# Performance work log

Hardware: AMD Instinct MI355X
Metric: run time of the kernel (lower is better)

## Reference

```python
import jax, jax.numpy as jnp
import numpy as np

DIM = 128       # model dim d
NEXP = 64       # number of experts
K = 2           # top-k (hardcoded in the module)
B, S = 1, 1024  # batch, seq
HID = DIM * 4   # expert FFN hidden = 4*d


def _gelu(v):
    # torch F.gelu / nn.GELU default = exact erf form
    return jax.nn.gelu(v, approximate=False)


def setup_inputs() -> dict:
    key = jax.random.key(0)
    ks = jax.random.split(key, 8)
    sc = 0.02
    xav = (2.0 / (HID + DIM)) ** 0.5  # xavier_normal std for [4d, d]
    x = jax.random.normal(ks[0], (B, S, DIM), jnp.float32)
    # gate MLP: Linear(d,4d) -> GELU -> Linear(4d,4d) -> GELU -> Linear(4d,E) -> Sigmoid
    gw1 = jax.random.normal(ks[1], (DIM, HID), jnp.float32) * sc
    gb1 = jnp.zeros((HID,), jnp.float32)
    gw2 = jax.random.normal(ks[2], (HID, HID), jnp.float32) * sc
    gb2 = jnp.zeros((HID,), jnp.float32)
    gw3 = jax.random.normal(ks[3], (HID, NEXP), jnp.float32) * sc
    gb3 = jnp.zeros((NEXP,), jnp.float32)
    # expert banks (shapes fixed to the consistent 2-layer FFN reading)
    W1 = jax.random.normal(ks[4], (NEXP, HID, DIM), jnp.float32) * xav
    B1 = jnp.zeros((NEXP, HID), jnp.float32)
    W2 = jax.random.normal(ks[5], (NEXP, DIM, HID), jnp.float32) * xav
    B2 = jnp.zeros((NEXP, DIM), jnp.float32)
    return dict(x=x, gw1=gw1, gb1=gb1, gw2=gw2, gb2=gb2, gw3=gw3, gb3=gb3,
                W1=W1, B1=B1, W2=W2, B2=B2)


def reference(x, gw1, gb1, gw2, gb2, gw3, gb3, W1, B1, W2, B2):
    # gating network -> sigmoid scores over experts
    h = _gelu(x @ gw1 + gb1)
    h = _gelu(h @ gw2 + gb2)
    gate = jax.nn.sigmoid(h @ gw3 + gb3)                 # [B,S,E]
    values, idx = jax.lax.top_k(gate, K)                 # [B,S,K]
    values = values / jnp.sum(values, axis=-1, keepdims=True)
    # naive per-token gather of full expert weights (matches original access pattern)
    w1g = W1[idx]                                        # [B,S,K,HID,DIM]
    b1g = B1[idx]                                        # [B,S,K,HID]
    w2g = W2[idx]                                        # [B,S,K,DIM,HID]
    b2g = B2[idx]                                        # [B,S,K,DIM]
    t = _gelu(jnp.einsum('bskfd,bsd->bskf', w1g, x) + b1g)   # [B,S,K,HID]
    y = _gelu(jnp.einsum('bskdf,bskf->bskd', w2g, t) + b2g)  # [B,S,K,DIM]
    return jnp.sum(y * values[..., None], axis=-2)           # [B,S,DIM]
```

## Files before the change

### kernel.cpp

```cpp
#include <hip/hip_runtime.h>
#include <math.h>

#define NDIM 128
#define NHID 512
#define NEXPERT 64
#define NTOK 1024
#define NPAIR (NTOK * 2)

typedef __attribute__((ext_vector_type(8))) short short8_t;
typedef __attribute__((ext_vector_type(4))) float f32x4;

__device__ __forceinline__ float gelu_f(float v) {
    return 0.5f * v * (1.0f + erff(v * 0.7071067811865476f));
}
__device__ __forceinline__ unsigned short f2bf(float f) {
    union { float f; unsigned u; } v; v.f = f;
    unsigned r = v.u + 0x7FFFu + ((v.u >> 16) & 1u);
    return (unsigned short)(r >> 16);
}
__device__ __forceinline__ float bf2f(unsigned short h) {
    union { unsigned u; float f; } v; v.u = ((unsigned)h) << 16;
    return v.f;
}
__device__ __forceinline__ void split3(float f, short& ho, short& mo, short& lo) {
    const unsigned short h = f2bf(f);
    const float r1 = f - bf2f(h);
    const unsigned short m = f2bf(r1);
    const unsigned short l = f2bf(r1 - bf2f(m));
    ho = (short)h; mo = (short)m; lo = (short)l;
}

__global__ __launch_bounds__(256) void k_g1d2(
        const float* __restrict__ x, const float* __restrict__ gw1,
        const float* __restrict__ gw2, const float* __restrict__ gb1,
        unsigned short* __restrict__ G2h, unsigned short* __restrict__ G2m,
        unsigned short* __restrict__ G2l, unsigned short* __restrict__ Hh,
        unsigned short* __restrict__ Hm, unsigned short* __restrict__ Hl) {
    __shared__ __align__(16) char smem[58112];
    const int j = threadIdx.x;
    if (blockIdx.x >= 256) {
        float (*T)[65] = (float (*)[65])smem;
        const int u = blockIdx.x - 256;
        const int k0 = (u >> 3) * 64, n0 = (u & 7) * 64;
#pragma unroll
        for (int q = 0; q < 4; ++q) {
            const int idx = j + 256 * q;
            const int kr = idx >> 4, c4 = idx & 15;
            float4 v = *(const float4*)(gw2 + (size_t)(k0 + kr) * NHID + n0 + c4 * 4);
            T[kr][c4 * 4 + 0] = v.x; T[kr][c4 * 4 + 1] = v.y;
            T[kr][c4 * 4 + 2] = v.z; T[kr][c4 * 4 + 3] = v.w;
        }
        __syncthreads();
#pragma unroll
        for (int q = 0; q < 4; ++q) {
            const int idx = j + 256 * q;
            const int n = idx >> 4, k4 = idx & 15;
            short4 sh, sm, sl;
#pragma unroll
            for (int qq = 0; qq < 4; ++qq)
                split3(T[k4 * 4 + qq][n], (&sh.x)[qq], (&sm.x)[qq], (&sl.x)[qq]);
            const size_t o = (size_t)(n0 + n) * NHID + k0 + k4 * 4;
            *(short4*)(G2h + o) = sh;
            *(short4*)(G2m + o) = sm;
            *(short4*)(G2l + o) = sl;
        }
        return;
    }
    short (*Ahs)[32][72] = (short (*)[32][72])smem;
    short (*Bss)[64][72] = (short (*)[64][72])(smem + 13824);
    float (*T)[65] = (float (*)[65])(smem + 41472);
    const int u = blockIdx.x;
    const int m0 = (u >> 3) * 32, n0 = (u & 7) * 64;
    const int w = j >> 6, lane = j & 63;
    const int mt = w & 1, npair = w >> 1;
    const int lrow = lane & 15, lseg = lane >> 4;
    f32x4 acc[2];
    acc[0] = (f32x4){0.f, 0.f, 0.f, 0.f};
    acc[1] = (f32x4){0.f, 0.f, 0.f, 0.f};
    for (int kc = 0; kc < NDIM; kc += 64) {
        __syncthreads();
#pragma unroll
        for (int q = 0; q < 4; ++q) {
            const int idx = j + 256 * q;
            const int kr = idx >> 4, c4 = idx & 15;
            float4 v = *(const float4*)(gw1 + (size_t)(kc + kr) * NHID + n0 + c4 * 4);
            T[kr][c4 * 4 + 0] = v.x; T[kr][c4 * 4 + 1] = v.y;
            T[kr][c4 * 4 + 2] = v.z; T[kr][c4 * 4 + 3] = v.w;
        }
#pragma unroll
        for (int q = 0; q < 2; ++q) {
            const int idx = j + 256 * q;
            const int row = idx >> 4, c4 = idx & 15;
            float4 v = *(const float4*)(x + (size_t)(m0 + row) * NDIM + kc + c4 * 4);
            short4 sh, sm, sl;
#pragma unroll
            for (int qq = 0; qq < 4; ++qq)
                split3((&v.x)[qq], (&sh.x)[qq], (&sm.x)[qq], (&sl.x)[qq]);
            *(short4*)&Ahs[0][row][c4 * 4] = sh;
            *(short4*)&Ahs[1][row][c4 * 4] = sm;
            *(short4*)&Ahs[2][row][c4 * 4] = sl;
        }
        __syncthreads();
#pragma unroll
        for (int q = 0; q < 4; ++q) {
            const int idx = j + 256 * q;
            const int nn = idx >> 4, k4 = idx & 15;
            short4 sh, sm, sl;
#pragma unroll
            for (int qq = 0; qq < 4; ++qq)
                split3(T[k4 * 4 + qq][nn], (&sh.x)[qq], (&sm.x)[qq], (&sl.x)[qq]);
            *(short4*)&Bss[0][nn][k4 * 4] = sh;
            *(short4*)&Bss[1][nn][k4 * 4] = sm;
            *(short4*)&Bss[2][nn][k4 * 4] = sl;
        }
        __syncthreads();
#pragma unroll
        for (int ks = 0; ks < 2; ++ks) {
            const int ko = ks * 32 + lseg * 8;
            short8_t ah = *(short8_t*)&Ahs[0][mt * 16 + lrow][ko];
            short8_t am = *(short8_t*)&Ahs[1][mt * 16 + lrow][ko];
            short8_t al = *(short8_t*)&Ahs[2][mt * 16 + lrow][ko];
#pragma unroll
            for (int nt = 0; nt < 2; ++nt) {
                const int nr = (npair * 2 + nt) * 16 + lrow;
                short8_t bh = *(short8_t*)&Bss[0][nr][ko];
                short8_t bm = *(short8_t*)&Bss[1][nr][ko];
                short8_t bl = *(short8_t*)&Bss[2][nr][ko];
                acc[nt] = __builtin_amdgcn_mfma_f32_16x16x32_bf16(ah, bh, acc[nt], 0, 0, 0);
                acc[nt] = __builtin_amdgcn_mfma_f32_16x16x32_bf16(am, bh, acc[nt], 0, 0, 0);
                acc[nt] = __builtin_amdgcn_mfma_f32_16x16x32_bf16(ah, bm, acc[nt], 0, 0, 0);
                acc[nt] = __builtin_amdgcn_mfma_f32_16x16x32_bf16(al, bh, acc[nt], 0, 0, 0);
                acc[nt] = __builtin_amdgcn_mfma_f32_16x16x32_bf16(ah, bl, acc[nt], 0, 0, 0);
                acc[nt] = __builtin_amdgcn_mfma_f32_16x16x32_bf16(am, bm, acc[nt], 0, 0, 0);
            }
        }
    }
#pragma unroll
    for (int nt = 0; nt < 2; ++nt) {
        const int col = n0 + (npair * 2 + nt) * 16 + lrow;
        const float bb = gb1[col];
#pragma unroll
        for (int r = 0; r < 4; ++r) {
            const int row = m0 + mt * 16 + lseg * 4 + r;
            const float h = gelu_f(acc[nt][r] + bb);
            short hh, hm, hl;
            split3(h, hh, hm, hl);
            const size_t o = (size_t)row * NHID + col;
            Hh[o] = (unsigned short)hh; Hm[o] = (unsigned short)hm;
            Hl[o] = (unsigned short)hl;
        }
    }
}

__global__ __launch_bounds__(256) void k_gate2(
        const unsigned short* __restrict__ Ahp, const unsigned short* __restrict__ Amp,
        const unsigned short* __restrict__ Alp,
        const unsigned short* __restrict__ Bhp, const unsigned short* __restrict__ Bmp,
        const unsigned short* __restrict__ Blp,
        const float* __restrict__ gb2, float* __restrict__ h2) {
    __shared__ short Ahs[3][32][72];
    __shared__ short Bss[3][64][72];
    const int j = threadIdx.x;
    const int u = blockIdx.x;
    const int m0 = (u >> 3) * 32, n0 = (u & 7) * 64;
    const int w = j >> 6, lane = j & 63;
    const int mt = w & 1, npair = w >> 1;
    const int lrow = lane & 15, lseg = lane >> 4;
    const int K = NHID;
    f32x4 acc[2];
    acc[0] = (f32x4){0.f, 0.f, 0.f, 0.f};
    acc[1] = (f32x4){0.f, 0.f, 0.f, 0.f};
    for (int kc = 0; kc < K; kc += 64) {
        __syncthreads();
        {
            const int row = j >> 3, c8 = j & 7;
            const size_t o = (size_t)(m0 + row) * K + kc + c8 * 8;
            *(short8_t*)&Ahs[0][row][c8 * 8] = *(const short8_t*)(Ahp + o);
            *(short8_t*)&Ahs[1][row][c8 * 8] = *(const short8_t*)(Amp + o);
            *(short8_t*)&Ahs[2][row][c8 * 8] = *(const short8_t*)(Alp + o);
        }
#pragma unroll
        for (int q = 0; q < 2; ++q) {
            const int idx = j + 256 * q;
            const int nr = idx >> 3, c8 = idx & 7;
            const size_t o = (size_t)(n0 + nr) * K + kc + c8 * 8;
            *(short8_t*)&Bss[0][nr][c8 * 8] = *(const short8_t*)(Bhp + o);
            *(short8_t*)&Bss[1][nr][c8 * 8] = *(const short8_t*)(Bmp + o);
            *(short8_t*)&Bss[2][nr][c8 * 8] = *(const short8_t*)(Blp + o);
        }
        __syncthreads();
#pragma unroll
        for (int ks = 0; ks < 2; ++ks) {
            const int ko = ks * 32 + lseg * 8;
            short8_t ah = *(short8_t*)&Ahs[0][mt * 16 + lrow][ko];
            short8_t am = *(short8_t*)&Ahs[1][mt * 16 + lrow][ko];
            short8_t al = *(short8_t*)&Ahs[2][mt * 16 + lrow][ko];
#pragma unroll
            for (int nt = 0; nt < 2; ++nt) {
                const int nr = (npair * 2 + nt) * 16 + lrow;
                short8_t bh = *(short8_t*)&Bss[0][nr][ko];
                short8_t bm = *(short8_t*)&Bss[1][nr][ko];
                short8_t bl = *(short8_t*)&Bss[2][nr][ko];
                acc[nt] = __builtin_amdgcn_mfma_f32_16x16x32_bf16(ah, bh, acc[nt], 0, 0, 0);
                acc[nt] = __builtin_amdgcn_mfma_f32_16x16x32_bf16(am, bh, acc[nt], 0, 0, 0);
                acc[nt] = __builtin_amdgcn_mfma_f32_16x16x32_bf16(ah, bm, acc[nt], 0, 0, 0);
                acc[nt] = __builtin_amdgcn_mfma_f32_16x16x32_bf16(al, bh, acc[nt], 0, 0, 0);
                acc[nt] = __builtin_amdgcn_mfma_f32_16x16x32_bf16(ah, bl, acc[nt], 0, 0, 0);
                acc[nt] = __builtin_amdgcn_mfma_f32_16x16x32_bf16(am, bm, acc[nt], 0, 0, 0);
            }
        }
    }
#pragma unroll
    for (int nt = 0; nt < 2; ++nt) {
        const int col = n0 + (npair * 2 + nt) * 16 + lrow;
        const float bb = gb2[col];
#pragma unroll
        for (int r = 0; r < 4; ++r) {
            const int row = m0 + mt * 16 + lseg * 4 + r;
            h2[(size_t)row * NHID + col] = gelu_f(acc[nt][r] + bb);
        }
    }
}

__global__ __launch_bounds__(256) void k_gate3(
        const float* __restrict__ h2, const float* __restrict__ gw3,
        const float* __restrict__ gb3, int* __restrict__ eidx,
        float* __restrict__ wval) {
    __shared__ float hs[8][132];
    __shared__ float gs[128][72];
    const int j = threadIdx.x;
    const int lane = j & 63;
    const int w = j >> 6;
    const int t0 = blockIdx.x * 8;
    float acc[2] = {0.f, 0.f};
    for (int k0 = 0; k0 < NHID; k0 += 128) {
        __syncthreads();
        {
            const int tok = j >> 5, c4 = j & 31;
            *(float4*)&hs[tok][c4 * 4] =
                *(const float4*)(h2 + (size_t)(t0 + tok) * NHID + k0 + c4 * 4);
        }
#pragma unroll
        for (int q = 0; q < 8; ++q) {
            const int idx = j + 256 * q;
            const int kk = idx >> 4, c4 = idx & 15;
            *(float4*)&gs[kk][c4 * 4] =
                *(const float4*)(gw3 + (size_t)(k0 + kk) * NEXPERT + c4 * 4);
        }
        __syncthreads();
        for (int kk = 0; kk < 128; ++kk) {
            const float g = gs[kk][lane];
            acc[0] += hs[w * 2][kk] * g;
            acc[1] += hs[w * 2 + 1][kk] * g;
        }
    }
    const float bias = gb3[lane];
#pragma unroll
    for (int i = 0; i < 2; ++i) {
        const int t = t0 + w * 2 + i;
        float s = 1.f / (1.f + expf(-(acc[i] + bias)));
        float v = s; int ix = lane;
#pragma unroll
        for (int off = 32; off >= 1; off >>= 1) {
            float ov = __shfl_xor(v, off);
            int oi = __shfl_xor(ix, off);
            if (ov > v || (ov == v && oi < ix)) { v = ov; ix = oi; }
        }
        const float v0 = v; const int i0 = ix;
        float v2 = (lane == i0) ? -1.f : s; int ix2 = lane;
#pragma unroll
        for (int off = 32; off >= 1; off >>= 1) {
            float ov = __shfl_xor(v2, off);
            int oi = __shfl_xor(ix2, off);
            if (ov > v2 || (ov == v2 && oi < ix2)) { v2 = ov; ix2 = oi; }
        }
        if (lane == 0) {
            float inv = 1.f / (v0 + v2);
            eidx[t * 2] = i0;  eidx[t * 2 + 1] = ix2;
            wval[t * 2] = v0 * inv;  wval[t * 2 + 1] = v2 * inv;
        }
    }
}

__device__ __forceinline__ int build_list(
        const int* __restrict__ eidx, int e, int lane, int w,
        int* lst, int* wtot) {
    unsigned long long msk[8];
    const int b0 = w * 512;
    int tot = 0;
#pragma unroll
    for (int c = 0; c < 8; ++c) {
        const int i = b0 + c * 64 + lane;
        msk[c] = __ballot(eidx[i] == e);
        tot += (int)__popcll(msk[c]);
    }
    if (lane == 0) wtot[w] = tot;
    __syncthreads();
    int woff = 0;
    for (int q = 0; q < w; ++q) woff += wtot[q];
    int run = 0;
#pragma unroll
    for (int c = 0; c < 8; ++c) {
        const int i = b0 + c * 64 + lane;
        if ((msk[c] >> lane) & 1ull)
            lst[woff + run + (int)__popcll(msk[c] & ((1ull << lane) - 1ull))] = i;
        run += (int)__popcll(msk[c]);
    }
    const int n = wtot[0] + wtot[1] + wtot[2] + wtot[3];
    __syncthreads();
    return n;
}

__global__ __launch_bounds__(256) void k_l1(
        const float* __restrict__ x, const float* __restrict__ W1,
        const float* __restrict__ B1, const int* __restrict__ eidx,
        unsigned short* __restrict__ tbuf) {
    __shared__ short As_[32 * 136];
    __shared__ short Bs_[64 * 136];
    __shared__ int prs[32];
    __shared__ int wtot[4];
    __shared__ int lst[NPAIR];
    const int j = threadIdx.x;
    const int lane = j & 63;
    const int w = j >> 6;
    const int e = blockIdx.x >> 3;
    const int f0 = (blockIdx.x & 7) * 64;
    char* Asc = (char*)As_;
    char* Bsc = (char*)Bs_;
    const int n = build_list(eidx, e, lane, w, lst, wtot);
    const float* W1e = W1 + (size_t)e * NHID * NDIM;
    for (int idx = j; idx < 2048; idx += 256) {
        const int f = idx >> 5, c4 = idx & 31;
        float4 v = *(const float4*)(W1e + (size_t)(f0 + f) * NDIM + c4 * 4);
        short4 s; s.x = (short)f2bf(v.x); s.y = (short)f2bf(v.y);
        s.z = (short)f2bf(v.z); s.w = (short)f2bf(v.w);
        *(short4*)(Bsc + f * 272 + c4 * 8) = s;
    }
    const float bbias = B1[e * NHID + f0 + w * 16 + (lane & 15)];
    for (int bt = 0; bt * 32 < n; ++bt) {
        __syncthreads();
        if (j < 32) prs[j] = (bt * 32 + j < n) ? lst[bt * 32 + j] : -1;
        __syncthreads();
        for (int idx = j; idx < 1024; idx += 256) {
            const int tok = idx >> 5, c4 = idx & 31;
            const int pr = prs[tok];
            float4 v = make_float4(0.f, 0.f, 0.f, 0.f);
            if (pr >= 0) v = ((const float4*)x)[(size_t)(pr >> 1) * 32 + c4];
            short4 s; s.x = (short)f2bf(v.x); s.y = (short)f2bf(v.y);
            s.z = (short)f2bf(v.z); s.w = (short)f2bf(v.w);
            *(short4*)(Asc + tok * 272 + c4 * 8) = s;
        }
        __syncthreads();
        f32x4 acc[2];
        acc[0] = (f32x4){0.f, 0.f, 0.f, 0.f};
        acc[1] = (f32x4){0.f, 0.f, 0.f, 0.f};
        const int acol = ((lane >> 4) << 4);
        const int brow = w * 16 + (lane & 15);
#pragma unroll
        for (int ks = 0; ks < 4; ++ks) {
            short8_t b = *(short8_t*)(Bsc + brow * 272 + ks * 64 + acol);
#pragma unroll
            for (int mt = 0; mt < 2; ++mt) {
                short8_t a = *(short8_t*)(Asc + (mt * 16 + (lane & 15)) * 272 + ks * 64 + acol);
                acc[mt] = __builtin_amdgcn_mfma_f32_16x16x32_bf16(a, b, acc[mt], 0, 0, 0);
            }
        }
        const int fcol = f0 + w * 16 + (lane & 15);
#pragma unroll
        for (int mt = 0; mt < 2; ++mt) {
#pragma unroll
            for (int r = 0; r < 4; ++r) {
                const int tok = mt * 16 + ((lane >> 4) << 2) + r;
                const int pr = prs[tok];
                if (pr >= 0)
                    tbuf[(size_t)pr * NHID + fcol] = f2bf(gelu_f(acc[mt][r] + bbias));
            }
        }
    }
}

__global__ __launch_bounds__(256) void k_l2(
        const float* __restrict__ W2, const int* __restrict__ eidx,
        const unsigned short* __restrict__ tbuf, float* __restrict__ pbuf) {
    __shared__ short As_[32 * 136];
    __shared__ short Bs_[64 * 136];
    __shared__ int prs[32];
    __shared__ int wtot[4];
    __shared__ int lst[NPAIR];
    const int j = threadIdx.x;
    const int lane = j & 63;
    const int w = j >> 6;
    const int e = blockIdx.x >> 3;
    const int d0 = ((blockIdx.x >> 2) & 1) * 64;
    const int kz = blockIdx.x & 3;
    const int k0 = kz * 128;
    char* Asc = (char*)As_;
    char* Bsc = (char*)Bs_;
    const int n = build_list(eidx, e, lane, w, lst, wtot);
    const float* W2e = W2 + (size_t)e * NDIM * NHID;
    for (int idx = j; idx < 2048; idx += 256) {
        const int d = idx >> 5, c4 = idx & 31;
        float4 v = *(const float4*)(W2e + (size_t)(d0 + d) * NHID + k0 + c4 * 4);
        short4 s; s.x = (short)f2bf(v.x); s.y = (short)f2bf(v.y);
        s.z = (short)f2bf(v.z); s.w = (short)f2bf(v.w);
        *(short4*)(Bsc + d * 272 + c4 * 8) = s;
    }
    float* pz = pbuf + (size_t)kz * NPAIR * NDIM;
    for (int bt = 0; bt * 32 < n; ++bt) {
        __syncthreads();
        if (j < 32) prs[j] = (bt * 32 + j < n) ? lst[bt * 32 + j] : -1;
        __syncthreads();
        for (int idx = j; idx < 512; idx += 256) {
            const int tok = idx >> 4, c8 = idx & 15;
            const int pr = prs[tok];
            short8_t v = (short8_t)(short)0;
            if (pr >= 0) v = *(const short8_t*)(tbuf + (size_t)pr * NHID + k0 + c8 * 8);
            *(short8_t*)(Asc + tok * 272 + c8 * 16) = v;
        }
        __syncthreads();
        f32x4 acc[2];
        acc[0] = (f32x4){0.f, 0.f, 0.f, 0.f};
        acc[1] = (f32x4){0.f, 0.f, 0.f, 0.f};
        const int acol = ((lane >> 4) << 4);
        const int brow = w * 16 + (lane & 15);
#pragma unroll
        for (int ks = 0; ks < 4; ++ks) {
            short8_t b = *(short8_t*)(Bsc + brow * 272 + ks * 64 + acol);
#pragma unroll
            for (int mt = 0; mt < 2; ++mt) {
                short8_t a = *(short8_t*)(Asc + (mt * 16 + (lane & 15)) * 272 + ks * 64 + acol);
                acc[mt] = __builtin_amdgcn_mfma_f32_16x16x32_bf16(a, b, acc[mt], 0, 0, 0);
            }
        }
        const int dcol = d0 + w * 16 + (lane & 15);
#pragma unroll
        for (int mt = 0; mt < 2; ++mt) {
#pragma unroll
            for (int r = 0; r < 4; ++r) {
                const int tok = mt * 16 + ((lane >> 4) << 2) + r;
                const int pr = prs[tok];
                if (pr >= 0) pz[(size_t)pr * NDIM + dcol] = acc[mt][r];
            }
        }
    }
}

__global__ __launch_bounds__(256) void k_combine(
        const float* __restrict__ pbuf, const float* __restrict__ wval,
        const int* __restrict__ eidx, const float* __restrict__ B2,
        float* __restrict__ out) {
    const int i = blockIdx.x * 256 + threadIdx.x;
    const int t = i >> 7, d = i & (NDIM - 1);
    const int KS = NPAIR * NDIM;
    float y[2];
#pragma unroll
    for (int k = 0; k < 2; ++k) {
        const int p = t * 2 + k;
        float s = pbuf[p * NDIM + d] + pbuf[KS + p * NDIM + d]
                + pbuf[2 * KS + p * NDIM + d] + pbuf[3 * KS + p * NDIM + d]
                + B2[eidx[p] * NDIM + d];
        y[k] = gelu_f(s);
    }
    out[i] = wval[t * 2] * y[0] + wval[t * 2 + 1] * y[1];
}

extern "C" void kernel_launch(void* const* d_in, const int* in_sizes, int n_in,
                              void* d_out, int out_size, void* d_ws, size_t ws_size,
                              hipStream_t stream) {
    const float* x   = (const float*)d_in[0];
    const float* gw1 = (const float*)d_in[1];
    const float* gb1 = (const float*)d_in[2];
    const float* gw2 = (const float*)d_in[3];
    const float* gb2 = (const float*)d_in[4];
    const float* gw3 = (const float*)d_in[5];
    const float* gb3 = (const float*)d_in[6];
    const float* W1  = (const float*)d_in[7];
    const float* B1  = (const float*)d_in[8];
    const float* W2  = (const float*)d_in[9];
    const float* B2  = (const float*)d_in[10];
    float* out = (float*)d_out;
    char* ws = (char*)d_ws;

    unsigned short* G2h = (unsigned short*)(ws);
    unsigned short* G2m = (unsigned short*)(ws + 524288);
    unsigned short* G2l = (unsigned short*)(ws + 1048576);
    unsigned short* Hh  = (unsigned short*)(ws + 1572864);
    unsigned short* Hm  = (unsigned short*)(ws + 2621440);
    unsigned short* Hl  = (unsigned short*)(ws + 3670016);
    float*          h2  = (float*)(ws + 4718592);
    unsigned short* tbuf = (unsigned short*)(ws);
    float*          pbuf = (float*)(ws + 2097152);
    int*   eidx = (int*)  (ws + 7340032);
    float* wval = (float*)(ws + 7340032 + 8192);

    k_g1d2<<<dim3(320), 256, 0, stream>>>(x, gw1, gw2, gb1, G2h, G2m, G2l, Hh, Hm, Hl);
    k_gate2<<<dim3(256), 256, 0, stream>>>(Hh, Hm, Hl, G2h, G2m, G2l, gb2, h2);
    k_gate3<<<dim3(128), 256, 0, stream>>>(h2, gw3, gb3, eidx, wval);
    k_l1<<<dim3(512), 256, 0, stream>>>(x, W1, B1, eidx, tbuf);
    k_l2<<<dim3(512), 256, 0, stream>>>(W2, eidx, tbuf, pbuf);
    k_combine<<<dim3(512), 256, 0, stream>>>(pbuf, wval, eidx, B2, out);
}
```

Measured before the change: 62.83 us.

## Fuse expert layer-1 and layer-2 kernels with per-expert spin barrier

```diff
diff --git a/kernel.cpp b/kernel.cpp
--- a/kernel.cpp
+++ b/kernel.cpp
@@ -225,17 +225,18 @@
 __global__ __launch_bounds__(256) void k_gate3(
         const float* __restrict__ h2, const float* __restrict__ gw3,
         const float* __restrict__ gb3, int* __restrict__ eidx,
-        float* __restrict__ wval) {
-    __shared__ float hs[8][132];
+        float* __restrict__ wval, int* __restrict__ cnt) {
+    __shared__ float hs[4][132];
     __shared__ float gs[128][72];
     const int j = threadIdx.x;
     const int lane = j & 63;
     const int w = j >> 6;
-    const int t0 = blockIdx.x * 8;
-    float acc[2] = {0.f, 0.f};
+    const int t0 = blockIdx.x * 4;
+    if (blockIdx.x == 0 && j < NEXPERT) cnt[j] = 0;
+    float acc = 0.f;
     for (int k0 = 0; k0 < NHID; k0 += 128) {
         __syncthreads();
-        {
+        if (j < 128) {
             const int tok = j >> 5, c4 = j & 31;
             *(float4*)&hs[tok][c4 * 4] =
                 *(const float4*)(h2 + (size_t)(t0 + tok) * NHID + k0 + c4 * 4);
@@ -248,17 +249,12 @@
                 *(const float4*)(gw3 + (size_t)(k0 + kk) * NEXPERT + c4 * 4);
         }
         __syncthreads();
-        for (int kk = 0; kk < 128; ++kk) {
-            const float g = gs[kk][lane];
-            acc[0] += hs[w * 2][kk] * g;
-            acc[1] += hs[w * 2 + 1][kk] * g;
-        }
+        for (int kk = 0; kk < 128; ++kk) acc += hs[w][kk] * gs[kk][lane];
     }
     const float bias = gb3[lane];
-#pragma unroll
-    for (int i = 0; i < 2; ++i) {
-        const int t = t0 + w * 2 + i;
-        float s = 1.f / (1.f + expf(-(acc[i] + bias)));
+    {
+        const int t = t0 + w;
+        float s = 1.f / (1.f + expf(-(acc + bias)));
         float v = s; int ix = lane;
 #pragma unroll
         for (int off = 32; off >= 1; off >>= 1) {
@@ -311,10 +307,11 @@
     return n;
 }
 
-__global__ __launch_bounds__(256) void k_l1(
+__global__ __launch_bounds__(256, 2) void k_l1l2(
         const float* __restrict__ x, const float* __restrict__ W1,
-        const float* __restrict__ B1, const int* __restrict__ eidx,
-        unsigned short* __restrict__ tbuf) {
+        const float* __restrict__ B1, const float* __restrict__ W2,
+        const int* __restrict__ eidx, unsigned short* __restrict__ tbuf,
+        float* __restrict__ pbuf, int* __restrict__ cnt) {
     __shared__ short As_[32 * 136];
     __shared__ short Bs_[64 * 136];
     __shared__ int prs[32];
@@ -323,123 +320,122 @@
     const int j = threadIdx.x;
     const int lane = j & 63;
     const int w = j >> 6;
-    const int e = blockIdx.x >> 3;
-    const int f0 = (blockIdx.x & 7) * 64;
+    const int e = blockIdx.x & 63;
+    const int u = blockIdx.x >> 6;
     char* Asc = (char*)As_;
     char* Bsc = (char*)Bs_;
     const int n = build_list(eidx, e, lane, w, lst, wtot);
-    const float* W1e = W1 + (size_t)e * NHID * NDIM;
-    for (int idx = j; idx < 2048; idx += 256) {
-        const int f = idx >> 5, c4 = idx & 31;
-        float4 v = *(const float4*)(W1e + (size_t)(f0 + f) * NDIM + c4 * 4);
-        short4 s; s.x = (short)f2bf(v.x); s.y = (short)f2bf(v.y);
-        s.z = (short)f2bf(v.z); s.w = (short)f2bf(v.w);
-        *(short4*)(Bsc + f * 272 + c4 * 8) = s;
-    }
-    const float bbias = B1[e * NHID + f0 + w * 16 + (lane & 15)];
-    for (int bt = 0; bt * 32 < n; ++bt) {
-        __syncthreads();
-        if (j < 32) prs[j] = (bt * 32 + j < n) ? lst[bt * 32 + j] : -1;
-        __syncthreads();
-        for (int idx = j; idx < 1024; idx += 256) {
-            const int tok = idx >> 5, c4 = idx & 31;
-            const int pr = prs[tok];
-            float4 v = make_float4(0.f, 0.f, 0.f, 0.f);
-            if (pr >= 0) v = ((const float4*)x)[(size_t)(pr >> 1) * 32 + c4];
+
+    {
+        const int f0 = u * 64;
+        const float* W1e = W1 + (size_t)e * NHID * NDIM;
+        for (int idx = j; idx < 2048; idx += 256) {
+            const int f = idx >> 5, c4 = idx & 31;
+            float4 v = *(const float4*)(W1e + (size_t)(f0 + f) * NDIM + c4 * 4);
             short4 s; s.x = (short)f2bf(v.x); s.y = (short)f2bf(v.y);
             s.z = (short)f2bf(v.z); s.w = (short)f2bf(v.w);
-            *(short4*)(Asc + tok * 272 + c4 * 8) = s;
-        }
-        __syncthreads();
-        f32x4 acc[2];
-        acc[0] = (f32x4){0.f, 0.f, 0.f, 0.f};
-        acc[1] = (f32x4){0.f, 0.f, 0.f, 0.f};
-        const int acol = ((lane >> 4) << 4);
-        const int brow = w * 16 + (lane & 15);
-#pragma unroll
-        for (int ks = 0; ks < 4; ++ks) {
-            short8_t b = *(short8_t*)(Bsc + brow * 272 + ks * 64 + acol);
+            *(short4*)(Bsc + f * 272 + c4 * 8) = s;
+        }
+        const float bbias = B1[e * NHID + f0 + w * 16 + (lane & 15)];
+        for (int bt = 0; bt * 32 < n; ++bt) {
+            __syncthreads();
+            if (j < 32) prs[j] = (bt * 32 + j < n) ? lst[bt * 32 + j] : -1;
+            __syncthreads();
+            for (int idx = j; idx < 1024; idx += 256) {
+                const int tok = idx >> 5, c4 = idx & 31;
+                const int pr = prs[tok];
+                float4 v = make_float4(0.f, 0.f, 0.f, 0.f);
+                if (pr >= 0) v = ((const float4*)x)[(size_t)(pr >> 1) * 32 + c4];
+                short4 s; s.x = (short)f2bf(v.x); s.y = (short)f2bf(v.y);
+                s.z = (short)f2bf(v.z); s.w = (short)f2bf(v.w);
+                *(short4*)(Asc + tok * 272 + c4 * 8) = s;
+            }
+            __syncthreads();
+            f32x4 acc[2];
+            acc[0] = (f32x4){0.f, 0.f, 0.f, 0.f};
+            acc[1] = (f32x4){0.f, 0.f, 0.f, 0.f};
+            const int acol = ((lane >> 4) << 4);
+            const int brow = w * 16 + (lane & 15);
+#pragma unroll
+            for (int ks = 0; ks < 4; ++ks) {
+                short8_t b = *(short8_t*)(Bsc + brow * 272 + ks * 64 + acol);
+#pragma unroll
+                for (int mt = 0; mt < 2; ++mt) {
+                    short8_t a = *(short8_t*)(Asc + (mt * 16 + (lane & 15)) * 272 + ks * 64 + acol);
+                    acc[mt] = __builtin_amdgcn_mfma_f32_16x16x32_bf16(a, b, acc[mt], 0, 0, 0);
+                }
+            }
+            const int fcol = f0 + w * 16 + (lane & 15);
 #pragma unroll
             for (int mt = 0; mt < 2; ++mt) {
-                short8_t a = *(short8_t*)(Asc + (mt * 16 + (lane & 15)) * 272 + ks * 64 + acol);
-                acc[mt] = __builtin_amdgcn_mfma_f32_16x16x32_bf16(a, b, acc[mt], 0, 0, 0);
-            }
-        }
-        const int fcol = f0 + w * 16 + (lane & 15);
-#pragma unroll
-        for (int mt = 0; mt < 2; ++mt) {
-#pragma unroll
-            for (int r = 0; r < 4; ++r) {
-                const int tok = mt * 16 + ((lane >> 4) << 2) + r;
+#pragma unroll
+                for (int r = 0; r < 4; ++r) {
+                    const int tok = mt * 16 + ((lane >> 4) << 2) + r;
+                    const int pr = prs[tok];
+                    if (pr >= 0)
+                        tbuf[(size_t)pr * NHID + fcol] = f2bf(gelu_f(acc[mt][r] + bbias));
+                }
+            }
+        }
+    }
+
+    __syncthreads();
+    if (j == 0) {
+        __threadfence();
+        atomicAdd(&cnt[e], 1);
+        while (atomicAdd(&cnt[e], 0) < 8) __builtin_amdgcn_s_sleep(16);
+    }
+    __syncthreads();
+    __threadfence();
+
+    {
+        const int d0 = (u & 1) * 64;
+        const int kz = u >> 1;
+        const int k0 = kz * 128;
+        const float* W2e = W2 + (size_t)e * NDIM * NHID;
+        for (int idx = j; idx < 2048; idx += 256) {
+            const int d = idx >> 5, c4 = idx & 31;
+            float4 v = *(const float4*)(W2e + (size_t)(d0 + d) * NHID + k0 + c4 * 4);
+            short4 s; s.x = (short)f2bf(v.x); s.y = (short)f2bf(v.y);
+            s.z = (short)f2bf(v.z); s.w = (short)f2bf(v.w);
+            *(short4*)(Bsc + d * 272 + c4 * 8) = s;
+        }
+        float* pz = pbuf + (size_t)kz * NPAIR * NDIM;
+        for (int bt = 0; bt * 32 < n; ++bt) {
+            __syncthreads();
+            if (j < 32) prs[j] = (bt * 32 + j < n) ? lst[bt * 32 + j] : -1;
+            __syncthreads();
+            for (int idx = j; idx < 512; idx += 256) {
+                const int tok = idx >> 4, c8 = idx & 15;
                 const int pr = prs[tok];
-                if (pr >= 0)
-                    tbuf[(size_t)pr * NHID + fcol] = f2bf(gelu_f(acc[mt][r] + bbias));
-            }
-        }
-    }
-}
-
-__global__ __launch_bounds__(256) void k_l2(
-        const float* __restrict__ W2, const int* __restrict__ eidx,
-        const unsigned short* __restrict__ tbuf, float* __restrict__ pbuf) {
-    __shared__ short As_[32 * 136];
-    __shared__ short Bs_[64 * 136];
-    __shared__ int prs[32];
-    __shared__ int wtot[4];
-    __shared__ int lst[NPAIR];
-    const int j = threadIdx.x;
-    const int lane = j & 63;
-    const int w = j >> 6;
-    const int e = blockIdx.x >> 3;
-    const int d0 = ((blockIdx.x >> 2) & 1) * 64;
-    const int kz = blockIdx.x & 3;
-    const int k0 = kz * 128;
-    char* Asc = (char*)As_;
-    char* Bsc = (char*)Bs_;
-    const int n = build_list(eidx, e, lane, w, lst, wtot);
-    const float* W2e = W2 + (size_t)e * NDIM * NHID;
-    for (int idx = j; idx < 2048; idx += 256) {
-        const int d = idx >> 5, c4 = idx & 31;
-        float4 v = *(const float4*)(W2e + (size_t)(d0 + d) * NHID + k0 + c4 * 4);
-        short4 s; s.x = (short)f2bf(v.x); s.y = (short)f2bf(v.y);
-        s.z = (short)f2bf(v.z); s.w = (short)f2bf(v.w);
-        *(short4*)(Bsc + d * 272 + c4 * 8) = s;
-    }
-    float* pz = pbuf + (size_t)kz * NPAIR * NDIM;
-    for (int bt = 0; bt * 32 < n; ++bt) {
-        __syncthreads();
-        if (j < 32) prs[j] = (bt * 32 + j < n) ? lst[bt * 32 + j] : -1;
-        __syncthreads();
-        for (int idx = j; idx < 512; idx += 256) {
-            const int tok = idx >> 4, c8 = idx & 15;
-            const int pr = prs[tok];
-            short8_t v = (short8_t)(short)0;
-            if (pr >= 0) v = *(const short8_t*)(tbuf + (size_t)pr * NHID + k0 + c8 * 8);
-            *(short8_t*)(Asc + tok * 272 + c8 * 16) = v;
-        }
-        __syncthreads();
-        f32x4 acc[2];
-        acc[0] = (f32x4){0.f, 0.f, 0.f, 0.f};
-        acc[1] = (f32x4){0.f, 0.f, 0.f, 0.f};
-        const int acol = ((lane >> 4) << 4);
-        const int brow = w * 16 + (lane & 15);
-#pragma unroll
-        for (int ks = 0; ks < 4; ++ks) {
-            short8_t b = *(short8_t*)(Bsc + brow * 272 + ks * 64 + acol);
+                short8_t v = (short8_t)(short)0;
+                if (pr >= 0) v = *(const short8_t*)(tbuf + (size_t)pr * NHID + k0 + c8 * 8);
+                *(short8_t*)(Asc + tok * 272 + c8 * 16) = v;
+            }
+            __syncthreads();
+            f32x4 acc[2];
+            acc[0] = (f32x4){0.f, 0.f, 0.f, 0.f};
+            acc[1] = (f32x4){0.f, 0.f, 0.f, 0.f};
+            const int acol = ((lane >> 4) << 4);
+            const int brow = w * 16 + (lane & 15);
+#pragma unroll
+            for (int ks = 0; ks < 4; ++ks) {
+                short8_t b = *(short8_t*)(Bsc + brow * 272 + ks * 64 + acol);
+#pragma unroll
+                for (int mt = 0; mt < 2; ++mt) {
+                    short8_t a = *(short8_t*)(Asc + (mt * 16 + (lane & 15)) * 272 + ks * 64 + acol);
+                    acc[mt] = __builtin_amdgcn_mfma_f32_16x16x32_bf16(a, b, acc[mt], 0, 0, 0);
+                }
+            }
+            const int dcol = d0 + w * 16 + (lane & 15);
 #pragma unroll
             for (int mt = 0; mt < 2; ++mt) {
-                short8_t a = *(short8_t*)(Asc + (mt * 16 + (lane & 15)) * 272 + ks * 64 + acol);
-                acc[mt] = __builtin_amdgcn_mfma_f32_16x16x32_bf16(a, b, acc[mt], 0, 0, 0);
-            }
-        }
-        const int dcol = d0 + w * 16 + (lane & 15);
-#pragma unroll
-        for (int mt = 0; mt < 2; ++mt) {
-#pragma unroll
-            for (int r = 0; r < 4; ++r) {
-                const int tok = mt * 16 + ((lane >> 4) << 2) + r;
-                const int pr = prs[tok];
-                if (pr >= 0) pz[(size_t)pr * NDIM + dcol] = acc[mt][r];
+#pragma unroll
+                for (int r = 0; r < 4; ++r) {
+                    const int tok = mt * 16 + ((lane >> 4) << 2) + r;
+                    const int pr = prs[tok];
+                    if (pr >= 0) pz[(size_t)pr * NDIM + dcol] = acc[mt][r];
+                }
             }
         }
     }
@@ -492,11 +488,11 @@
     float*          pbuf = (float*)(ws + 2097152);
     int*   eidx = (int*)  (ws + 7340032);
     float* wval = (float*)(ws + 7340032 + 8192);
+    int*   cnt  = (int*)  (ws + 7340032 + 16384);
 
     k_g1d2<<<dim3(320), 256, 0, stream>>>(x, gw1, gw2, gb1, G2h, G2m, G2l, Hh, Hm, Hl);
     k_gate2<<<dim3(256), 256, 0, stream>>>(Hh, Hm, Hl, G2h, G2m, G2l, gb2, h2);
-    k_gate3<<<dim3(128), 256, 0, stream>>>(h2, gw3, gb3, eidx, wval);
-    k_l1<<<dim3(512), 256, 0, stream>>>(x, W1, B1, eidx, tbuf);
-    k_l2<<<dim3(512), 256, 0, stream>>>(W2, eidx, tbuf, pbuf);
+    k_gate3<<<dim3(256), 256, 0, stream>>>(h2, gw3, gb3, eidx, wval, cnt);
+    k_l1l2<<<dim3(512), 256, 0, stream>>>(x, W1, B1, W2, eidx, tbuf, pbuf, cnt);
     k_combine<<<dim3(512), 256, 0, stream>>>(pbuf, wval, eidx, B2, out);
 }
```

Result: slower. 117.4 us (+86.8%).
